# Optimization experiments

Measured on AMD Instinct MI355X. Metric: run time of the kernel, lower is better.

## Reference

```python
import math
import jax, jax.numpy as jnp
import numpy as np

H, N2, B, L = 256, 32, 8, 4096
DT_MIN, DT_MAX = 1e-3, 1e-1

def setup_inputs() -> dict:
    key = jax.random.key(0)
    ks = jax.random.split(key, 6)
    u = jax.random.normal(ks[0], (B, H, L), dtype=jnp.float32)
    # log_dt uniform in [log(dt_min), log(dt_max)] as in S4DKernel.__init__
    log_dt = jax.random.uniform(ks[1], (H,), dtype=jnp.float32) * (
        math.log(DT_MAX) - math.log(DT_MIN)) + math.log(DT_MIN)
    C = jax.random.normal(ks[2], (H, N2, 2), dtype=jnp.float32)  # view_as_real of complex C
    log_A_real = jnp.log(0.5 * jnp.ones((H, N2), dtype=jnp.float32))
    A_imag = math.pi * jnp.broadcast_to(jnp.arange(N2, dtype=jnp.float32), (H, N2))
    D = jax.random.normal(ks[3], (H,), dtype=jnp.float32)
    W = jax.random.normal(ks[4], (2 * H, H), dtype=jnp.float32) / math.sqrt(H)
    b = jax.random.normal(ks[5], (2 * H,), dtype=jnp.float32) * 0.01
    return {"u": u, "log_dt": log_dt, "C": C, "log_A_real": log_A_real,
            "A_imag": A_imag, "D": D, "W": W, "b": b}

def reference(u, log_dt, C, log_A_real, A_imag, D, W, b):
    # ---- S4DKernel: generate convolution kernel k (H, L) ----
    Lk = u.shape[-1]
    dt = jnp.exp(log_dt)                                  # (H,)
    Cc = C[..., 0] + 1j * C[..., 1]                       # (H, N2) complex
    A = -jnp.exp(log_A_real) + 1j * A_imag                # (H, N2) complex
    dtA = A * dt[:, None]                                 # (H, N2)
    # Vandermonde: exp(dtA * l) for l in [0, L)  -> (H, N2, L) complex
    K = jnp.exp(dtA[:, :, None] * jnp.arange(Lk, dtype=jnp.float32))
    Ct = Cc * (jnp.exp(dtA) - 1.0) / A                    # (H, N2)
    k = 2.0 * jnp.einsum('hn,hnl->hl', Ct, K).real        # (H, L) float32
    # ---- FFT long convolution ----
    n = 2 * Lk
    k_f = jnp.fft.rfft(k, n=n)                            # (H, n//2+1)
    u_f = jnp.fft.rfft(u, n=n)                            # (B, H, n//2+1)
    y = jnp.fft.irfft(u_f * k_f, n=n)[..., :Lk]           # (B, H, L)
    y = y + u * D[:, None]                                # skip connection
    y = jax.nn.gelu(y, approximate=False)                 # nn.GELU (exact)
    # ---- output 1x1 conv (H -> 2H) + GLU over channel dim ----
    z = jnp.einsum('oh,bhl->bol', W, y) + b[None, :, None]  # (B, 2H, L)
    a, g = jnp.split(z, 2, axis=1)
    return a * jax.nn.sigmoid(g)                          # (B, H, L)
```

## Files before the change

kernel.cpp:

```cpp
#include <hip/hip_runtime.h>
#include <math.h>

#define H 256
#define N2 32
#define Bsz 8
#define Lseq 4096
#define BH (Bsz*H)
#define NCH 32
#define LC (Lseq/NCH)
#define HN (H*N2)

#define Y_OFF  0
#define WB_OFF (Y_OFF + (BH*Lseq/2))
#define TB_OFF (WB_OFF + (512*256/2))
#define EB_OFF (TB_OFF + (H*128*128/2))
#define VB_OFF (EB_OFF + (H*128*64/2))

typedef __attribute__((ext_vector_type(8))) short bf16x8;
typedef __attribute__((ext_vector_type(8))) unsigned short u16x8;
typedef __attribute__((ext_vector_type(4))) float f32x4;

__device__ __forceinline__ unsigned short f2bf(float x) {
  union { float f; unsigned int u; } v; v.f = x;
  unsigned int r = v.u + 0x7fffu + ((v.u >> 16) & 1u);
  return (unsigned short)(r >> 16);
}
__device__ __forceinline__ unsigned int packbf(float lo, float hi) {
  return (unsigned int)f2bf(lo) | ((unsigned int)f2bf(hi) << 16);
}
__device__ __forceinline__ float bf2f(unsigned short b) {
  union { unsigned int u; float f; } v; v.u = ((unsigned int)b) << 16;
  return v.f;
}

__global__ __launch_bounds__(128) void k_prep(const float* __restrict__ log_dt,
                                              const float* __restrict__ C,
                                              const float* __restrict__ lar,
                                              const float* __restrict__ aim,
                                              const float* __restrict__ W,
                                              unsigned short* __restrict__ Wb,
                                              unsigned short* __restrict__ Tb,
                                              unsigned short* __restrict__ Eb,
                                              unsigned short* __restrict__ Vb) {
  __shared__ unsigned short kbuf[128];
  int h = blockIdx.x;
  int j = threadIdx.x;
  {
    int i = h * 128 + j;
    float4 v = *(const float4*)&W[i * 4];
    uint2 p; p.x = packbf(v.x, v.y); p.y = packbf(v.z, v.w);
    *(uint2*)&Wb[i * 4] = p;
  }
  float dt = expf(log_dt[h]);
  float kacc = 0.f;
  unsigned short* Erow = Eb + (h * 128 + j) * 64;
  for (int n = 0; n < 32; n++) {
    int hn = (h << 5) + n;
    float Ar = -expf(lar[hn]), Ai = aim[hn];
    float dAr = Ar * dt, dAi = Ai * dt;
    float er = expf(dAr), sw, cw;
    sincosf(dAi, &sw, &cw);
    float wr = er * cw, wi = er * sw;
    float emr = wr - 1.f, emi = wi;
    float inv = 1.f / (Ar * Ar + Ai * Ai);
    float qr = (emr * Ar + emi * Ai) * inv;
    float qi = (emi * Ar - emr * Ai) * inv;
    float Cr = C[2 * hn], Ci = C[2 * hn + 1];
    float c2r = 2.f * (Cr * qr - Ci * qi);
    float c2i = 2.f * (Cr * qi + Ci * qr);
    float ej = expf(dAr * (float)j), sj, cj;
    sincosf(dAi * (float)j, &sj, &cj);
    kacc = fmaf(c2r, ej * cj, fmaf(-c2i, ej * sj, kacc));
    float e1 = expf(dAr * (float)(j + 1)), s1, c1;
    sincosf(dAi * (float)(j + 1), &s1, &c1);
    float w1r = e1 * c1, w1i = e1 * s1;
    Erow[2 * n]     = f2bf(c2r * w1r - c2i * w1i);
    Erow[2 * n + 1] = f2bf(-(c2r * w1i + c2i * w1r));
    float ev = expf(dAr * (float)(127 - j)), sv, cv;
    sincosf(dAi * (float)(127 - j), &sv, &cv);
    Vb[(h * 64 + 2 * n) * 128 + j]     = f2bf(ev * cv);
    Vb[(h * 64 + 2 * n + 1) * 128 + j] = f2bf(ev * sv);
  }
  kbuf[j] = f2bf(kacc);
  __syncthreads();
  unsigned short* Trow = Tb + (h * 128 + j) * 128;
#pragma unroll
  for (int s8 = 0; s8 < 16; s8++) {
    u16x8 v;
#pragma unroll
    for (int t = 0; t < 8; t++) {
      int m = s8 * 8 + t;
      v[t] = (j >= m) ? kbuf[j - m] : (unsigned short)0;
    }
    *(u16x8*)&Trow[s8 * 8] = v;
  }
}

__global__ __launch_bounds__(256) void k_ssm(const float* __restrict__ u,
                                             const float* __restrict__ log_dt,
                                             const float* __restrict__ lar,
                                             const float* __restrict__ aim,
                                             const unsigned short* __restrict__ Vb,
                                             const unsigned short* __restrict__ Tb,
                                             const unsigned short* __restrict__ Eb,
                                             const float* __restrict__ Dp,
                                             unsigned short* __restrict__ yb) {
  __shared__ unsigned short Ub[32][136];
  __shared__ float          Fb[32][68];
  __shared__ unsigned short Fl[32][72];
  int g   = blockIdx.x;
  int b   = g & 7, h = g >> 3;
  int tid = threadIdx.x;
  int wv = tid >> 6, lane = tid & 63;
  int n16 = lane & 15, quad = lane >> 4;
  const float* ubase = u + (b * 256 + h) * 4096;

#pragma unroll
  for (int i = 0; i < 2; i++) {
    int idx = tid * 2 + i;
    float4 va = *(const float4*)(ubase + idx * 8);
    float4 vb4 = *(const float4*)(ubase + idx * 8 + 4);
    unsigned short* dst = &Ub[idx >> 4][(idx & 15) * 8];
    *(unsigned int*)(dst)     = packbf(va.x, va.y);
    *(unsigned int*)(dst + 2) = packbf(va.z, va.w);
    *(unsigned int*)(dst + 4) = packbf(vb4.x, vb4.y);
    *(unsigned int*)(dst + 6) = packbf(vb4.z, vb4.w);
  }
  __syncthreads();

  {
    f32x4 sacc[2] = {};
#pragma unroll
    for (int ks = 0; ks < 128; ks += 32) {
      int kc = ks + quad * 8;
      bf16x8 bv = *(const bf16x8*)&Vb[(h * 64 + wv * 16 + n16) * 128 + kc];
#pragma unroll
      for (int mt = 0; mt < 2; mt++) {
        bf16x8 av = *(const bf16x8*)&Ub[mt * 16 + n16][kc];
        sacc[mt] = __builtin_amdgcn_mfma_f32_16x16x32_bf16(av, bv, sacc[mt], 0, 0, 0);
      }
    }
#pragma unroll
    for (int mt = 0; mt < 2; mt++)
#pragma unroll
      for (int reg = 0; reg < 4; reg++)
        Fb[mt * 16 + quad * 4 + reg][wv * 16 + n16] = sacc[mt][reg];
  }
  __syncthreads();

  if (wv == 0 && lane < 32) {
    int n = lane, hn = (h << 5) + n;
    float dt  = expf(log_dt[h]);
    float dAr = -expf(lar[hn]) * dt, dAi = aim[hn] * dt;
    float eL = expf(dAr * (float)LC), sL, cL;
    sincosf(dAi * (float)LC, &sL, &cL);
    float wLr = eL * cL, wLi = eL * sL;
    float fr = 0.f, fi = 0.f;
    for (int c = 0; c < NCH; c++) {
      float sr = Fb[c][2 * n], si = Fb[c][2 * n + 1];
      *(unsigned int*)&Fl[c][2 * n] = packbf(fr, fi);
      float nr = fmaf(wLr, fr, fmaf(-wLi, fi, sr));
      float ni = fmaf(wLr, fi, fmaf(wLi, fr, si));
      fr = nr; fi = ni;
    }
  }
  __syncthreads();

  f32x4 acc[2][2] = {};
#pragma unroll
  for (int ks = 0; ks < 192; ks += 32) {
    int kc = ks + quad * 8;
    bf16x8 av[2];
#pragma unroll
    for (int mt = 0; mt < 2; mt++)
      av[mt] = (ks < 128) ? *(const bf16x8*)&Ub[mt * 16 + n16][kc]
                          : *(const bf16x8*)&Fl[mt * 16 + n16][kc - 128];
#pragma unroll
    for (int ntl = 0; ntl < 2; ntl++) {
      int j = (wv * 2 + ntl) * 16 + n16;
      bf16x8 bv = (ks < 128) ? *(const bf16x8*)&Tb[(h * 128 + j) * 128 + kc]
                             : *(const bf16x8*)&Eb[(h * 128 + j) * 64 + kc - 128];
#pragma unroll
      for (int mt = 0; mt < 2; mt++)
        acc[mt][ntl] = __builtin_amdgcn_mfma_f32_16x16x32_bf16(av[mt], bv, acc[mt][ntl], 0, 0, 0);
    }
  }

  float Dh = Dp[h];
  unsigned short* ybase = yb + (b * 256 + h) * 4096;
#pragma unroll
  for (int mt = 0; mt < 2; mt++) {
#pragma unroll
    for (int reg = 0; reg < 4; reg++) {
      int c = mt * 16 + quad * 4 + reg;
#pragma unroll
      for (int ntl = 0; ntl < 2; ntl++) {
        int j = (wv * 2 + ntl) * 16 + n16;
        float uv = bf2f(Ub[c][j]);
        float v  = fmaf(Dh, uv, acc[mt][ntl][reg]);
        float ge = 0.5f * v * (1.0f + erff(v * 0.70710678118654752f));
        ybase[c * 128 + j] = f2bf(ge);
      }
    }
  }
}

__global__ __launch_bounds__(256) void k_gemm(const unsigned short* __restrict__ yb,
                                              const unsigned short* __restrict__ Wb,
                                              const float* __restrict__ bias,
                                              float* __restrict__ out) {
  __shared__ unsigned short Ws[128][72];
  __shared__ unsigned short Ys[128][72];
  int tid  = threadIdx.x;
  int l0   = blockIdx.x * 128;
  int o0   = blockIdx.y * 64;
  int bb   = blockIdx.z;
  int wave = tid >> 6;
  int lane = tid & 63;
  int wo   = wave & 1;
  int wl   = wave >> 1;
  int n    = lane & 15;
  int quad = lane >> 4;

  f32x4 acc_a[2][4] = {};
  f32x4 acc_g[2][4] = {};

  for (int kk = 0; kk < H; kk += 64) {
#pragma unroll
    for (int i = 0; i < 4; i++) {
      int e = tid + i * 256;
      int r = e >> 3, s = e & 7;
      int gr = (r < 64) ? (o0 + r) : (192 + o0 + r);
      *(u16x8*)&Ws[r][s * 8] = *(const u16x8*)&Wb[gr * 256 + kk + s * 8];
    }
    {
      int kcol = tid & 63;
      int lg0  = tid >> 6;
      const unsigned short* yrow = yb + (bb * 256 + kk + kcol) * 4096 + l0;
#pragma unroll
      for (int i = 0; i < 4; i++) {
        int l8 = (lg0 * 4 + i) * 8;
        u16x8 v = *(const u16x8*)&yrow[l8];
#pragma unroll
        for (int jj = 0; jj < 8; jj++)
          Ys[l8 + jj][kcol] = v[jj];
      }
    }
    __syncthreads();
#pragma unroll
    for (int ks = 0; ks < 64; ks += 32) {
      int kc = ks + quad * 8;
      bf16x8 af_a[2], af_g[2], bfr[4];
#pragma unroll
      for (int mt = 0; mt < 2; mt++) {
        af_a[mt] = *(const bf16x8*)&Ws[wo * 32 + mt * 16 + n][kc];
        af_g[mt] = *(const bf16x8*)&Ws[64 + wo * 32 + mt * 16 + n][kc];
      }
#pragma unroll
      for (int lt = 0; lt < 4; lt++)
        bfr[lt] = *(const bf16x8*)&Ys[wl * 64 + lt * 16 + n][kc];
#pragma unroll
      for (int mt = 0; mt < 2; mt++)
#pragma unroll
        for (int lt = 0; lt < 4; lt++) {
          acc_a[mt][lt] = __builtin_amdgcn_mfma_f32_16x16x32_bf16(af_a[mt], bfr[lt], acc_a[mt][lt], 0, 0, 0);
          acc_g[mt][lt] = __builtin_amdgcn_mfma_f32_16x16x32_bf16(af_g[mt], bfr[lt], acc_g[mt][lt], 0, 0, 0);
        }
    }
    __syncthreads();
  }
#pragma unroll
  for (int mt = 0; mt < 2; mt++) {
    int ob = o0 + wo * 32 + mt * 16 + quad * 4;
#pragma unroll
    for (int reg = 0; reg < 4; reg++) {
      int op = ob + reg;
      float ba = bias[op], bg = bias[H + op];
      float* orow = &out[(bb * H + op) * Lseq + l0 + wl * 64 + n];
#pragma unroll
      for (int lt = 0; lt < 4; lt++) {
        float a = acc_a[mt][lt][reg] + ba;
        float g = acc_g[mt][lt][reg] + bg;
        orow[lt * 16] = a / (1.0f + expf(-g));
      }
    }
  }
}

extern "C" void kernel_launch(void* const* d_in, const int* in_sizes, int n_in,
                              void* d_out, int out_size, void* d_ws, size_t ws_size,
                              hipStream_t stream) {
  const float* u      = (const float*)d_in[0];
  const float* log_dt = (const float*)d_in[1];
  const float* C      = (const float*)d_in[2];
  const float* lar    = (const float*)d_in[3];
  const float* aim    = (const float*)d_in[4];
  const float* Dp     = (const float*)d_in[5];
  const float* W      = (const float*)d_in[6];
  const float* bias   = (const float*)d_in[7];
  float* out = (float*)d_out;
  float* ws  = (float*)d_ws;
  unsigned short* yb  = (unsigned short*)(ws + Y_OFF);
  unsigned short* Wb  = (unsigned short*)(ws + WB_OFF);
  unsigned short* Tbg = (unsigned short*)(ws + TB_OFF);
  unsigned short* Ebg = (unsigned short*)(ws + EB_OFF);
  unsigned short* Vbg = (unsigned short*)(ws + VB_OFF);

  hipLaunchKernelGGL(k_prep, dim3(H), dim3(128), 0, stream, log_dt, C, lar, aim, W, Wb, Tbg, Ebg, Vbg);
  hipLaunchKernelGGL(k_ssm,  dim3(BH), dim3(256), 0, stream, u, log_dt, lar, aim, Vbg, Tbg, Ebg, Dp, yb);
  hipLaunchKernelGGL(k_gemm, dim3(Lseq / 128, H / 64, Bsz), dim3(256), 0, stream, yb, Wb, bias, out);
}
```

Baseline: 167.6 us.

## Parallelize prep over modes, keep u in registers, double-buffer GEMM Y tiles

k_prep now runs 512 threads per head, splitting the 32 modes across four groups and reducing the partial kernel sums through shared memory, which raises parallelism in the prep stage. k_ssm loads u straight from global memory into register MFMA fragments instead of staging it in LDS, reorders block indices so blocks adjacent in launch order share batch and differ in head, and replaces exact erf GELU with the tanh approximation written as a sigmoid. k_gemm double-buffers the Y tile with register prefetch, drops one barrier per k-step, and reads W fragments directly from global memory instead of LDS. The tanh-form GELU changes the numerics slightly relative to the exact reference.

After: 168.1 us. No clear change (+0.3%).

```diff
diff --git a/kernel.cpp b/kernel.cpp
--- a/kernel.cpp
+++ b/kernel.cpp
@@ -33,7 +33,7 @@
   return v.f;
 }
 
-__global__ __launch_bounds__(128) void k_prep(const float* __restrict__ log_dt,
+__global__ __launch_bounds__(512) void k_prep(const float* __restrict__ log_dt,
                                               const float* __restrict__ C,
                                               const float* __restrict__ lar,
                                               const float* __restrict__ aim,
@@ -42,11 +42,14 @@
                                               unsigned short* __restrict__ Tb,
                                               unsigned short* __restrict__ Eb,
                                               unsigned short* __restrict__ Vb) {
+  __shared__ float kpart[3][128];
   __shared__ unsigned short kbuf[128];
-  int h = blockIdx.x;
-  int j = threadIdx.x;
-  {
-    int i = h * 128 + j;
+  int h   = blockIdx.x;
+  int tid = threadIdx.x;
+  int j   = tid & 127;
+  int ng  = tid >> 7;
+  if (tid < 128) {
+    int i = h * 128 + tid;
     float4 v = *(const float4*)&W[i * 4];
     uint2 p; p.x = packbf(v.x, v.y); p.y = packbf(v.z, v.w);
     *(uint2*)&Wb[i * 4] = p;
@@ -54,7 +57,8 @@
   float dt = expf(log_dt[h]);
   float kacc = 0.f;
   unsigned short* Erow = Eb + (h * 128 + j) * 64;
-  for (int n = 0; n < 32; n++) {
+  for (int nn = 0; nn < 8; nn++) {
+    int n  = ng * 8 + nn;
     int hn = (h << 5) + n;
     float Ar = -expf(lar[hn]), Ai = aim[hn];
     float dAr = Ar * dt, dAi = Ai * dt;
@@ -81,11 +85,14 @@
     Vb[(h * 64 + 2 * n) * 128 + j]     = f2bf(ev * cv);
     Vb[(h * 64 + 2 * n + 1) * 128 + j] = f2bf(ev * sv);
   }
-  kbuf[j] = f2bf(kacc);
+  if (ng) kpart[ng - 1][j] = kacc;
+  __syncthreads();
+  if (ng == 0) kbuf[j] = f2bf(kacc + kpart[0][j] + kpart[1][j] + kpart[2][j]);
   __syncthreads();
   unsigned short* Trow = Tb + (h * 128 + j) * 128;
 #pragma unroll
-  for (int s8 = 0; s8 < 16; s8++) {
+  for (int s8i = 0; s8i < 4; s8i++) {
+    int s8 = ng * 4 + s8i;
     u16x8 v;
 #pragma unroll
     for (int t = 0; t < 8; t++) {
@@ -105,40 +112,39 @@
                                              const unsigned short* __restrict__ Eb,
                                              const float* __restrict__ Dp,
                                              unsigned short* __restrict__ yb) {
-  __shared__ unsigned short Ub[32][136];
   __shared__ float          Fb[32][68];
   __shared__ unsigned short Fl[32][72];
   int g   = blockIdx.x;
-  int b   = g & 7, h = g >> 3;
+  int h   = g & 255, b = g >> 8;
   int tid = threadIdx.x;
   int wv = tid >> 6, lane = tid & 63;
   int n16 = lane & 15, quad = lane >> 4;
   const float* ubase = u + (b * 256 + h) * 4096;
 
-#pragma unroll
-  for (int i = 0; i < 2; i++) {
-    int idx = tid * 2 + i;
-    float4 va = *(const float4*)(ubase + idx * 8);
-    float4 vb4 = *(const float4*)(ubase + idx * 8 + 4);
-    unsigned short* dst = &Ub[idx >> 4][(idx & 15) * 8];
-    *(unsigned int*)(dst)     = packbf(va.x, va.y);
-    *(unsigned int*)(dst + 2) = packbf(va.z, va.w);
-    *(unsigned int*)(dst + 4) = packbf(vb4.x, vb4.y);
-    *(unsigned int*)(dst + 6) = packbf(vb4.z, vb4.w);
-  }
-  __syncthreads();
+  bf16x8 av[4][2];
+#pragma unroll
+  for (int ksi = 0; ksi < 4; ksi++) {
+#pragma unroll
+    for (int mt = 0; mt < 2; mt++) {
+      const float* p = ubase + (mt * 16 + n16) * 128 + ksi * 32 + quad * 8;
+      float4 a4 = *(const float4*)p;
+      float4 b4 = *(const float4*)(p + 4);
+      union { bf16x8 v; unsigned int w[4]; } t;
+      t.w[0] = packbf(a4.x, a4.y); t.w[1] = packbf(a4.z, a4.w);
+      t.w[2] = packbf(b4.x, b4.y); t.w[3] = packbf(b4.z, b4.w);
+      av[ksi][mt] = t.v;
+    }
+  }
 
   {
     f32x4 sacc[2] = {};
 #pragma unroll
-    for (int ks = 0; ks < 128; ks += 32) {
-      int kc = ks + quad * 8;
+    for (int ksi = 0; ksi < 4; ksi++) {
+      int kc = ksi * 32 + quad * 8;
       bf16x8 bv = *(const bf16x8*)&Vb[(h * 64 + wv * 16 + n16) * 128 + kc];
 #pragma unroll
-      for (int mt = 0; mt < 2; mt++) {
-        bf16x8 av = *(const bf16x8*)&Ub[mt * 16 + n16][kc];
-        sacc[mt] = __builtin_amdgcn_mfma_f32_16x16x32_bf16(av, bv, sacc[mt], 0, 0, 0);
-      }
+      for (int mt = 0; mt < 2; mt++)
+        sacc[mt] = __builtin_amdgcn_mfma_f32_16x16x32_bf16(av[ksi][mt], bv, sacc[mt], 0, 0, 0);
     }
 #pragma unroll
     for (int mt = 0; mt < 2; mt++)
@@ -168,21 +174,21 @@
 
   f32x4 acc[2][2] = {};
 #pragma unroll
-  for (int ks = 0; ks < 192; ks += 32) {
-    int kc = ks + quad * 8;
-    bf16x8 av[2];
+  for (int ksi = 0; ksi < 6; ksi++) {
+    int kc = ksi * 32 + quad * 8;
+    bf16x8 a2[2];
 #pragma unroll
     for (int mt = 0; mt < 2; mt++)
-      av[mt] = (ks < 128) ? *(const bf16x8*)&Ub[mt * 16 + n16][kc]
-                          : *(const bf16x8*)&Fl[mt * 16 + n16][kc - 128];
+      a2[mt] = (ksi < 4) ? av[ksi][mt]
+                         : *(const bf16x8*)&Fl[mt * 16 + n16][kc - 128];
 #pragma unroll
     for (int ntl = 0; ntl < 2; ntl++) {
       int j = (wv * 2 + ntl) * 16 + n16;
-      bf16x8 bv = (ks < 128) ? *(const bf16x8*)&Tb[(h * 128 + j) * 128 + kc]
-                             : *(const bf16x8*)&Eb[(h * 128 + j) * 64 + kc - 128];
+      bf16x8 bv = (ksi < 4) ? *(const bf16x8*)&Tb[(h * 128 + j) * 128 + kc]
+                            : *(const bf16x8*)&Eb[(h * 128 + j) * 64 + kc - 128];
 #pragma unroll
       for (int mt = 0; mt < 2; mt++)
-        acc[mt][ntl] = __builtin_amdgcn_mfma_f32_16x16x32_bf16(av[mt], bv, acc[mt][ntl], 0, 0, 0);
+        acc[mt][ntl] = __builtin_amdgcn_mfma_f32_16x16x32_bf16(a2[mt], bv, acc[mt][ntl], 0, 0, 0);
     }
   }
 
@@ -196,9 +202,10 @@
 #pragma unroll
       for (int ntl = 0; ntl < 2; ntl++) {
         int j = (wv * 2 + ntl) * 16 + n16;
-        float uv = bf2f(Ub[c][j]);
+        float uv = ubase[c * 128 + j];
         float v  = fmaf(Dh, uv, acc[mt][ntl][reg]);
-        float ge = 0.5f * v * (1.0f + erff(v * 0.70710678118654752f));
+        float t2 = 1.5957691216057308f * v * fmaf(0.044715f, v * v, 1.0f);
+        float ge = v / (1.0f + expf(-t2));
         ybase[c * 128 + j] = f2bf(ge);
       }
     }
@@ -209,8 +216,7 @@
                                               const unsigned short* __restrict__ Wb,
                                               const float* __restrict__ bias,
                                               float* __restrict__ out) {
-  __shared__ unsigned short Ws[128][72];
-  __shared__ unsigned short Ys[128][72];
+  __shared__ unsigned short Ys[2][128][72];
   int tid  = threadIdx.x;
   int l0   = blockIdx.x * 128;
   int o0   = blockIdx.y * 64;
@@ -221,44 +227,50 @@
   int wl   = wave >> 1;
   int n    = lane & 15;
   int quad = lane >> 4;
+  int kcol = tid & 63;
+  int lg0  = tid >> 6;
 
   f32x4 acc_a[2][4] = {};
   f32x4 acc_g[2][4] = {};
 
+  u16x8 yreg[4];
+  {
+    const unsigned short* yr = yb + (size_t)(bb * 256 + kcol) * 4096 + l0;
+#pragma unroll
+    for (int i = 0; i < 4; i++)
+      yreg[i] = *(const u16x8*)&yr[(lg0 * 4 + i) * 8];
+  }
+
+#pragma unroll
   for (int kk = 0; kk < H; kk += 64) {
+    int cur = (kk >> 6) & 1;
 #pragma unroll
     for (int i = 0; i < 4; i++) {
-      int e = tid + i * 256;
-      int r = e >> 3, s = e & 7;
-      int gr = (r < 64) ? (o0 + r) : (192 + o0 + r);
-      *(u16x8*)&Ws[r][s * 8] = *(const u16x8*)&Wb[gr * 256 + kk + s * 8];
-    }
-    {
-      int kcol = tid & 63;
-      int lg0  = tid >> 6;
-      const unsigned short* yrow = yb + (bb * 256 + kk + kcol) * 4096 + l0;
-#pragma unroll
-      for (int i = 0; i < 4; i++) {
-        int l8 = (lg0 * 4 + i) * 8;
-        u16x8 v = *(const u16x8*)&yrow[l8];
-#pragma unroll
-        for (int jj = 0; jj < 8; jj++)
-          Ys[l8 + jj][kcol] = v[jj];
-      }
+      int l8 = (lg0 * 4 + i) * 8;
+#pragma unroll
+      for (int jj = 0; jj < 8; jj++)
+        Ys[cur][l8 + jj][kcol] = yreg[i][jj];
     }
     __syncthreads();
+    if (kk + 64 < H) {
+      const unsigned short* yr = yb + (size_t)(bb * 256 + kk + 64 + kcol) * 4096 + l0;
+#pragma unroll
+      for (int i = 0; i < 4; i++)
+        yreg[i] = *(const u16x8*)&yr[(lg0 * 4 + i) * 8];
+    }
 #pragma unroll
     for (int ks = 0; ks < 64; ks += 32) {
       int kc = ks + quad * 8;
       bf16x8 af_a[2], af_g[2], bfr[4];
 #pragma unroll
       for (int mt = 0; mt < 2; mt++) {
-        af_a[mt] = *(const bf16x8*)&Ws[wo * 32 + mt * 16 + n][kc];
-        af_g[mt] = *(const bf16x8*)&Ws[64 + wo * 32 + mt * 16 + n][kc];
+        int oa = o0 + wo * 32 + mt * 16 + n;
+        af_a[mt] = *(const bf16x8*)&Wb[(size_t)oa * 256 + kk + kc];
+        af_g[mt] = *(const bf16x8*)&Wb[(size_t)(256 + oa) * 256 + kk + kc];
       }
 #pragma unroll
       for (int lt = 0; lt < 4; lt++)
-        bfr[lt] = *(const bf16x8*)&Ys[wl * 64 + lt * 16 + n][kc];
+        bfr[lt] = *(const bf16x8*)&Ys[cur][wl * 64 + lt * 16 + n][kc];
 #pragma unroll
       for (int mt = 0; mt < 2; mt++)
 #pragma unroll
@@ -267,7 +279,6 @@
           acc_g[mt][lt] = __builtin_amdgcn_mfma_f32_16x16x32_bf16(af_g[mt], bfr[lt], acc_g[mt][lt], 0, 0, 0);
         }
     }
-    __syncthreads();
   }
 #pragma unroll
   for (int mt = 0; mt < 2; mt++) {
@@ -280,8 +291,8 @@
 #pragma unroll
       for (int lt = 0; lt < 4; lt++) {
         float a = acc_a[mt][lt][reg] + ba;
-        float g = acc_g[mt][lt][reg] + bg;
-        orow[lt * 16] = a / (1.0f + expf(-g));
+        float gg = acc_g[mt][lt][reg] + bg;
+        orow[lt * 16] = a / (1.0f + expf(-gg));
       }
     }
   }
@@ -306,7 +317,7 @@
   unsigned short* Ebg = (unsigned short*)(ws + EB_OFF);
   unsigned short* Vbg = (unsigned short*)(ws + VB_OFF);
 
-  hipLaunchKernelGGL(k_prep, dim3(H), dim3(128), 0, stream, log_dt, C, lar, aim, W, Wb, Tbg, Ebg, Vbg);
+  hipLaunchKernelGGL(k_prep, dim3(H), dim3(512), 0, stream, log_dt, C, lar, aim, W, Wb, Tbg, Ebg, Vbg);
   hipLaunchKernelGGL(k_ssm,  dim3(BH), dim3(256), 0, stream, u, log_dt, lar, aim, Vbg, Tbg, Ebg, Dp, yb);
   hipLaunchKernelGGL(k_gemm, dim3(Lseq / 128, H / 64, Bsz), dim3(256), 0, stream, yb, Wb, bias, out);
 }
```
